# Performance work log

Measured on AMD Instinct MI355X. Metric: run time of the kernel, lower is better.

The kernel has to match this reference:

```python
import jax, jax.numpy as jnp
import numpy as np

B, S, D = 1, 2048, 2048
N_HEADS, N_KV_HEADS = 32, 8
HEAD_DIM = D // N_HEADS  # 64
N_REP = N_HEADS // N_KV_HEADS  # 4


def setup_inputs() -> dict:
    key = jax.random.key(0)
    ks = jax.random.split(key, 6)
    x = jax.random.normal(ks[0], (B, S, D), dtype=jnp.float32)
    # weights stored as [in, out] so projection is x @ W
    wq = jax.random.normal(ks[1], (D, N_HEADS * HEAD_DIM), dtype=jnp.float32) * 0.02
    wk = jax.random.normal(ks[2], (D, N_KV_HEADS * HEAD_DIM), dtype=jnp.float32) * 0.02
    wv = jax.random.normal(ks[3], (D, N_KV_HEADS * HEAD_DIM), dtype=jnp.float32) * 0.02
    wo = jax.random.normal(ks[4], (N_HEADS * HEAD_DIM, D), dtype=jnp.float32) * 0.02
    # RoPE tables: freqs_cis has shape (seqlen, head_dim//2)
    theta = 10000.0
    inv_freq = 1.0 / (theta ** (jnp.arange(0, HEAD_DIM, 2, dtype=jnp.float32) / HEAD_DIM))
    angles = jnp.arange(S, dtype=jnp.float32)[:, None] * inv_freq[None, :]  # [S, hd/2]
    freqs_cos = jnp.cos(angles)
    freqs_sin = jnp.sin(angles)
    # causal additive mask, broadcast to [b, h, q, k]
    mask = jnp.triu(jnp.full((S, S), -jnp.inf, dtype=jnp.float32), k=1)[None, None]
    return {"x": x, "wq": wq, "wk": wk, "wv": wv, "wo": wo,
            "freqs_cos": freqs_cos, "freqs_sin": freqs_sin, "mask": mask}


def _apply_rope(t, cos, sin):
    # t: [B, S, H, head_dim]; pairs (t[...,2i], t[...,2i+1]) form complex numbers
    tr = t[..., 0::2]
    ti = t[..., 1::2]
    c = cos[None, :, None, :]
    s = sin[None, :, None, :]
    out_r = tr * c - ti * s
    out_i = tr * s + ti * c
    return jnp.stack([out_r, out_i], axis=-1).reshape(t.shape)


def reference(x, wq, wk, wv, wo, freqs_cos, freqs_sin, mask):
    bsz, seqlen, _ = x.shape
    xq = (x @ wq).reshape(bsz, seqlen, N_HEADS, HEAD_DIM)
    xk = (x @ wk).reshape(bsz, seqlen, N_KV_HEADS, HEAD_DIM)
    xv = (x @ wv).reshape(bsz, seqlen, N_KV_HEADS, HEAD_DIM)
    xq = _apply_rope(xq, freqs_cos, freqs_sin)
    xk = _apply_rope(xk, freqs_cos, freqs_sin)
    # repeat_kv (GQA expansion): [b,s,kvh,d] -> [b,s,h,d]
    keys = jnp.repeat(xk, N_REP, axis=2)
    values = jnp.repeat(xv, N_REP, axis=2)
    scale = 1.0 / np.sqrt(HEAD_DIM)
    # scores: [b, h, q, k]
    scores = jnp.einsum('bqhd,bkhd->bhqk', xq, keys) * scale
    scores = scores + mask
    probs = jax.nn.softmax(scores.astype(jnp.float32), axis=-1).astype(x.dtype)
    out = jnp.einsum('bhqk,bkhd->bqhd', probs, values)
    out = out.reshape(bsz, seqlen, N_HEADS * HEAD_DIM)
    return out @ wo
```

## Files before the change

kernel.cpp:

```cpp
#include <hip/hip_runtime.h>
#include <hip/hip_bf16.h>

#define S_LEN 2048
#define D_MODEL 2048
#define N_HEADS 32
#define N_KV 8
#define HEAD_DIM 64
#define KV_DIM (N_KV * HEAD_DIM)
#define QKV_N (D_MODEL + 2 * KV_DIM)

typedef __bf16 bf16_t;
typedef __attribute__((ext_vector_type(8))) __bf16 bf16x8;
typedef __attribute__((ext_vector_type(4))) float f32x4;
typedef __attribute__((ext_vector_type(16))) float f32x16;
typedef __attribute__((ext_vector_type(4))) unsigned int uint4v;
typedef __attribute__((ext_vector_type(2))) unsigned int uint2v;

__device__ __forceinline__ void gload_lds16(const void* g, void* l) {
    __builtin_amdgcn_global_load_lds(
        (const __attribute__((address_space(1))) unsigned char*)g,
        (__attribute__((address_space(3))) unsigned char*)l,
        16, 0, 0);
}

__global__ __launch_bounds__(256) void transpose_convert(const float* __restrict__ src,
                                                         __hip_bfloat16* __restrict__ dst,
                                                         int R, int C) {
    __shared__ float tile[32][33];
    const int bx = blockIdx.x * 32;
    const int by = blockIdx.y * 32;
    const int tx = threadIdx.x;
    const int ty = threadIdx.y;
#pragma unroll
    for (int i = 0; i < 32; i += 8)
        tile[ty + i][tx] = src[(size_t)(by + ty + i) * C + bx + tx];
    __syncthreads();
#pragma unroll
    for (int i = 0; i < 32; i += 8)
        dst[(size_t)(bx + ty + i) * R + by + tx] = __float2bfloat16(tile[tx][ty + i]);
}

__global__ __launch_bounds__(256) void convert_bf16(const float* __restrict__ src,
                                                    __hip_bfloat16* __restrict__ dst) {
    const int i = (blockIdx.x * 256 + threadIdx.x) * 8;
    const float4 a = *reinterpret_cast<const float4*>(src + i);
    const float4 b = *reinterpret_cast<const float4*>(src + i + 4);
    bf16x8 r;
    r[0] = (__bf16)a.x; r[1] = (__bf16)a.y; r[2] = (__bf16)a.z; r[3] = (__bf16)a.w;
    r[4] = (__bf16)b.x; r[5] = (__bf16)b.y; r[6] = (__bf16)b.z; r[7] = (__bf16)b.w;
    *reinterpret_cast<bf16x8*>(dst + i) = r;
}

__global__ __launch_bounds__(256) void rope_qk(__hip_bfloat16* __restrict__ t,
                                               const float* __restrict__ cos_t,
                                               const float* __restrict__ sin_t) {
    const int idx = blockIdx.x * blockDim.x + threadIdx.x;
    const int i = idx & 31;
    const int hh = (idx >> 5) % (N_HEADS + N_KV);
    const int s = idx / (32 * (N_HEADS + N_KV));
    const float c = cos_t[s * 32 + i];
    const float sn = sin_t[s * 32 + i];
    int col; float scale;
    if (hh < N_HEADS) { col = hh * HEAD_DIM + 2 * i; scale = 0.125f * 1.44269504f; }
    else { col = D_MODEL + (hh - N_HEADS) * HEAD_DIM + 2 * i; scale = 1.0f; }
    __hip_bfloat16* p = &t[(size_t)s * QKV_N + col];
    const float re = __bfloat162float(p[0]);
    const float im = __bfloat162float(p[1]);
    p[0] = __float2bfloat16((re * c - im * sn) * scale);
    p[1] = __float2bfloat16((re * sn + im * c) * scale);
}

__global__ __launch_bounds__(256) void transpose_v(const __hip_bfloat16* __restrict__ QKV,
                                                   __hip_bfloat16* __restrict__ Vt) {
    __shared__ __align__(16) __bf16 tile[64][72];
    const int s0 = blockIdx.x * 64;
    const int hkv = blockIdx.y;
    const int tid = threadIdx.x;
    {
        const int r = tid >> 2;
        const int c0 = (tid & 3) * 16;
        const __hip_bfloat16* src = QKV + (size_t)(s0 + r) * QKV_N + D_MODEL + KV_DIM + hkv * HEAD_DIM + c0;
        *reinterpret_cast<bf16x8*>(&tile[r][c0]) = *reinterpret_cast<const bf16x8*>(src);
        *reinterpret_cast<bf16x8*>(&tile[r][c0 + 8]) = *reinterpret_cast<const bf16x8*>(src + 8);
    }
    __syncthreads();
    {
        const int d = tid >> 2;
        const int sc = (tid & 3) * 16;
        bf16x8 o0, o1;
#pragma unroll
        for (int j = 0; j < 8; ++j) { o0[j] = tile[sc + j][d]; o1[j] = tile[sc + 8 + j][d]; }
        __hip_bfloat16* dst = Vt + (size_t)(hkv * HEAD_DIM + d) * S_LEN + s0 + sc;
        *reinterpret_cast<bf16x8*>(dst) = o0;
        *reinterpret_cast<bf16x8*>(dst + 8) = o1;
    }
}

__device__ inline void storeC(__hip_bfloat16* p, float v) { *p = __float2bfloat16(v); }
__device__ inline void storeC(float* p, float v) { *p = v; }

template <typename OutT>
__global__ __launch_bounds__(256) void gemm_bt(const __hip_bfloat16* __restrict__ A,
                                               const __hip_bfloat16* __restrict__ Bt,
                                               OutT* __restrict__ C,
                                               int M, int N, int K) {
    __shared__ __align__(16) __bf16 As[2][128 * 32];
    __shared__ __align__(16) __bf16 Bs[2][128 * 32];
    const int tid = threadIdx.x;
    const int w = tid >> 6, l = tid & 63;
    const int wr = w >> 1, wc = w & 1;
    const int l4 = l >> 4, l15 = l & 15;
    const int bm = blockIdx.y * 128, bn = blockIdx.x * 128;

    f32x4 acc[4][4];
#pragma unroll
    for (int i = 0; i < 4; ++i)
#pragma unroll
        for (int j = 0; j < 4; ++j) acc[i][j] = (f32x4){0.f, 0.f, 0.f, 0.f};

    const int r0 = tid >> 2;
    const int cc0 = tid & 3;

    auto stage = [&](int buf, int k0) {
#pragma unroll
        for (int p = 0; p < 2; ++p) {
            const int row = p * 64 + r0;
            const int cs = cc0 ^ (row & 3);
            gload_lds16(&A[(size_t)(bm + row) * K + k0 + cs * 8], &As[buf][(p * 256 + tid) * 8]);
            gload_lds16(&Bt[(size_t)(bn + row) * K + k0 + cs * 8], &Bs[buf][(p * 256 + tid) * 8]);
        }
    };

    const int nk = K >> 5;
    stage(0, 0);
    asm volatile("s_waitcnt vmcnt(0)" ::: "memory");
    __builtin_amdgcn_s_barrier();

#pragma unroll 2
    for (int kt = 0; kt < nk; ++kt) {
        const int cur = kt & 1;
        if (kt + 1 < nk) stage(cur ^ 1, (kt + 1) * 32);
        bf16x8 a[4], b[4];
#pragma unroll
        for (int mi = 0; mi < 4; ++mi) {
            const int rr = wr * 64 + mi * 16 + l15;
            a[mi] = *reinterpret_cast<const bf16x8*>(&As[cur][rr * 32 + ((l4 ^ (rr & 3))) * 8]);
        }
#pragma unroll
        for (int ni = 0; ni < 4; ++ni) {
            const int rr = wc * 64 + ni * 16 + l15;
            b[ni] = *reinterpret_cast<const bf16x8*>(&Bs[cur][rr * 32 + ((l4 ^ (rr & 3))) * 8]);
        }
#pragma unroll
        for (int mi = 0; mi < 4; ++mi)
#pragma unroll
            for (int ni = 0; ni < 4; ++ni)
                acc[mi][ni] = __builtin_amdgcn_mfma_f32_16x16x32_bf16(a[mi], b[ni], acc[mi][ni], 0, 0, 0);
        asm volatile("s_waitcnt vmcnt(0)" ::: "memory");
        __builtin_amdgcn_s_barrier();
    }
#pragma unroll
    for (int mi = 0; mi < 4; ++mi)
#pragma unroll
        for (int ni = 0; ni < 4; ++ni)
#pragma unroll
            for (int r = 0; r < 4; ++r) {
                const int row = bm + wr * 64 + mi * 16 + l4 * 4 + r;
                const int col = bn + wc * 64 + ni * 16 + l15;
                storeC(&C[(size_t)row * N + col], acc[mi][ni][r]);
            }
}

__device__ __forceinline__ unsigned cvtpk_bf16(float lo, float hi) {
    unsigned w;
    asm("v_cvt_pk_bf16_f32 %0, %1, %2" : "=v"(w) : "v"(lo), "v"(hi));
    return w;
}
template <int R0>
__device__ __forceinline__ bf16x8 build_pfrag(const f32x16& s, int hi) {
    const unsigned A0 = cvtpk_bf16(s[R0 + 0], s[R0 + 1]);
    const unsigned A1 = cvtpk_bf16(s[R0 + 2], s[R0 + 3]);
    const unsigned B0 = cvtpk_bf16(s[R0 + 4], s[R0 + 5]);
    const unsigned B1 = cvtpk_bf16(s[R0 + 6], s[R0 + 7]);
    const unsigned pA0 = __shfl_xor(A0, 32, 64);
    const unsigned pA1 = __shfl_xor(A1, 32, 64);
    const unsigned pB0 = __shfl_xor(B0, 32, 64);
    const unsigned pB1 = __shfl_xor(B1, 32, 64);
    uint4v u;
    u[0] = hi ? pB0 : A0;
    u[1] = hi ? pB1 : A1;
    u[2] = hi ? B0 : pA0;
    u[3] = hi ? B1 : pA1;
    return __builtin_bit_cast(bf16x8, u);
}

__global__ __launch_bounds__(512) void attn_kernel(const __hip_bfloat16* __restrict__ QKV,
                                                   const __hip_bfloat16* __restrict__ Vt,
                                                   __hip_bfloat16* __restrict__ O,
                                                   float* __restrict__ Opart,
                                                   float* __restrict__ ms,
                                                   int split) {
    const int h = blockIdx.y;
    const int hkv = h >> 2;
    int qc = 0, sl = 0, gbase = 0, ns = 1;
    if (!split) {
        qc = 7 - (int)blockIdx.x;
    } else {
        const int x = (int)blockIdx.x;
        int cum = 0;
#pragma unroll
        for (int q = 0; q < 8; ++q) {
            const int n = (q + 2) >> 1;
            if (x >= cum && x < cum + n) { qc = q; sl = x - cum; gbase = cum; }
            cum += n;
        }
        ns = (qc + 2) >> 1;
    }
    const int ntf = 4 * (qc + 1);
    const int t0 = split ? sl * 8 : 0;
    const int t1 = split ? min(t0 + 8, ntf) : ntf;

    const int tid = threadIdx.x;
    const int w = tid >> 6, l = tid & 63;
    const int lq = l & 31, hi = l >> 5;
    const int q0w = qc * 256 + w * 32;
    const int qlane = q0w + lq;

    __shared__ __align__(16) __bf16 Ks[2][64 * 64];
    __shared__ __align__(16) __bf16 Vs[2][64 * 64];

    const __hip_bfloat16* Kg = QKV + D_MODEL + hkv * HEAD_DIM;
    const __hip_bfloat16* Vg = Vt + (size_t)hkv * HEAD_DIM * S_LEN;

    auto stage = [&](int buf, int kv0) {
        const int chunk = tid;
        const int r = chunk >> 3;
        const int cs = (chunk & 7) ^ (r & 7);
        gload_lds16(&Kg[(size_t)(kv0 + r) * QKV_N + cs * 8], &Ks[buf][chunk * 8]);
        gload_lds16(&Vg[(size_t)r * S_LEN + kv0 + cs * 8], &Vs[buf][chunk * 8]);
    };

    bf16x8 qf[4];
#pragma unroll
    for (int f = 0; f < 4; ++f)
        qf[f] = *reinterpret_cast<const bf16x8*>(
            &QKV[(size_t)qlane * QKV_N + h * HEAD_DIM + 16 * f + 8 * hi]);

    f32x16 o0, o1;
#pragma unroll
    for (int r = 0; r < 16; ++r) { o0[r] = 0.f; o1[r] = 0.f; }
    float m_run = -__builtin_inff(), s_run = 0.f;

    stage(0, t0 * 64);

#pragma unroll 1
    for (int t = t0; t < t1; ++t) {
        __syncthreads();
        if (t + 1 < t1) stage((t + 1 - t0) & 1, (t + 1) * 64);
        const int kv0 = t * 64;
        if (kv0 <= q0w + 31) {
            const __bf16* Kb = Ks[(t - t0) & 1];
            const __bf16* Vb = Vs[(t - t0) & 1];

            f32x16 s0, s1;
#pragma unroll
            for (int r = 0; r < 16; ++r) { s0[r] = 0.f; s1[r] = 0.f; }
#pragma unroll
            for (int f = 0; f < 4; ++f) {
                const int rr0 = lq;
                const int rr1 = 32 + lq;
                const bf16x8 ka0 = *reinterpret_cast<const bf16x8*>(
                    &Kb[rr0 * 64 + (((2 * f + hi) ^ (rr0 & 7))) * 8]);
                const bf16x8 ka1 = *reinterpret_cast<const bf16x8*>(
                    &Kb[rr1 * 64 + (((2 * f + hi) ^ (rr1 & 7))) * 8]);
                s0 = __builtin_amdgcn_mfma_f32_32x32x16_bf16(ka0, qf[f], s0, 0, 0, 0);
                s1 = __builtin_amdgcn_mfma_f32_32x32x16_bf16(ka1, qf[f], s1, 0, 0, 0);
            }
            if (kv0 + 63 > q0w) {
#pragma unroll
                for (int r = 0; r < 16; ++r) {
                    const int kvb = (r & 3) + 8 * (r >> 2) + 4 * hi;
                    if (kv0 + kvb > qlane) s0[r] = -__builtin_inff();
                    if (kv0 + 32 + kvb > qlane) s1[r] = -__builtin_inff();
                }
            }
            float ta = fmaxf(s0[0], s1[0]), tb = fmaxf(s0[1], s1[1]);
            float tc = fmaxf(s0[2], s1[2]), td = fmaxf(s0[3], s1[3]);
#pragma unroll
            for (int r = 4; r < 16; r += 4) {
                ta = fmaxf(ta, fmaxf(s0[r], s1[r]));
                tb = fmaxf(tb, fmaxf(s0[r + 1], s1[r + 1]));
                tc = fmaxf(tc, fmaxf(s0[r + 2], s1[r + 2]));
                td = fmaxf(td, fmaxf(s0[r + 3], s1[r + 3]));
            }
            float m_row = fmaxf(fmaxf(ta, tb), fmaxf(tc, td));
            m_row = fmaxf(m_row, __shfl_xor(m_row, 32, 64));

            if (!__all(m_row <= m_run + 8.0f)) {
                const float mnew = fmaxf(m_run, m_row);
                const float corr = exp2f(m_run - mnew);
                m_run = mnew;
                s_run *= corr;
#pragma unroll
                for (int r = 0; r < 16; ++r) { o0[r] *= corr; o1[r] *= corr; }
            }
#pragma unroll
            for (int r = 0; r < 16; ++r) {
                s0[r] = exp2f(s0[r] - m_run);
                s1[r] = exp2f(s1[r] - m_run);
            }
            float ua = s0[0] + s1[0], ub = s0[1] + s1[1];
            float uc = s0[2] + s1[2], ud = s0[3] + s1[3];
#pragma unroll
            for (int r = 4; r < 16; r += 4) {
                ua += s0[r] + s1[r];
                ub += s0[r + 1] + s1[r + 1];
                uc += s0[r + 2] + s1[r + 2];
                ud += s0[r + 3] + s1[r + 3];
            }
            float rs = (ua + ub) + (uc + ud);
            rs += __shfl_xor(rs, 32, 64);
            s_run += rs;

            bf16x8 pa[4];
            pa[0] = build_pfrag<0>(s0, hi);
            pa[1] = build_pfrag<8>(s0, hi);
            pa[2] = build_pfrag<0>(s1, hi);
            pa[3] = build_pfrag<8>(s1, hi);

#pragma unroll
            for (int ks = 0; ks < 4; ++ks) {
                const int rv0 = lq;
                const int rv1 = 32 + lq;
                const bf16x8 va0 = *reinterpret_cast<const bf16x8*>(
                    &Vb[rv0 * 64 + (((2 * ks + hi) ^ (rv0 & 7))) * 8]);
                const bf16x8 va1 = *reinterpret_cast<const bf16x8*>(
                    &Vb[rv1 * 64 + (((2 * ks + hi) ^ (rv1 & 7))) * 8]);
                o0 = __builtin_amdgcn_mfma_f32_32x32x16_bf16(va0, pa[ks], o0, 0, 0, 0);
                o1 = __builtin_amdgcn_mfma_f32_32x32x16_bf16(va1, pa[ks], o1, 0, 0, 0);
            }
        }
    }

    if (ns == 1) {
        const float inv = 1.0f / s_run;
        __hip_bfloat16* orow = O + (size_t)qlane * D_MODEL + h * HEAD_DIM;
#pragma unroll
        for (int rr = 0; rr < 4; ++rr) {
            {
                uint2v u;
                u[0] = cvtpk_bf16(o0[4 * rr] * inv, o0[4 * rr + 1] * inv);
                u[1] = cvtpk_bf16(o0[4 * rr + 2] * inv, o0[4 * rr + 3] * inv);
                *reinterpret_cast<uint2v*>(orow + 8 * rr + 4 * hi) = u;
            }
            {
                uint2v u;
                u[0] = cvtpk_bf16(o1[4 * rr] * inv, o1[4 * rr + 1] * inv);
                u[1] = cvtpk_bf16(o1[4 * rr + 2] * inv, o1[4 * rr + 3] * inv);
                *reinterpret_cast<uint2v*>(orow + 32 + 8 * rr + 4 * hi) = u;
            }
        }
    } else {
        const int g = h * 20 + gbase + sl;
        const int row = w * 32 + lq;
        const size_t base = ((size_t)g * 256 + row) * 64;
#pragma unroll
        for (int rr = 0; rr < 4; ++rr) {
            f32x4 v0, v1;
#pragma unroll
            for (int j = 0; j < 4; ++j) { v0[j] = o0[4 * rr + j]; v1[j] = o1[4 * rr + j]; }
            *reinterpret_cast<f32x4*>(&Opart[base + 8 * rr + 4 * hi]) = v0;
            *reinterpret_cast<f32x4*>(&Opart[base + 32 + 8 * rr + 4 * hi]) = v1;
        }
        if (hi == 0) {
            const size_t mi = (size_t)g * 256 + row;
            ms[mi * 2] = m_run;
            ms[mi * 2 + 1] = s_run;
        }
    }
}

__device__ __constant__ int kCum[8] = {0, 1, 2, 4, 6, 9, 12, 16};

__global__ __launch_bounds__(256) void attn_merge(const float* __restrict__ Opart,
                                                  const float* __restrict__ ms,
                                                  __hip_bfloat16* __restrict__ O) {
    const int qc = 2 + blockIdx.x;
    const int h = blockIdx.z;
    const int tid = threadIdx.x;
    const int row = blockIdx.y * 32 + (tid >> 3);
    const int dv0 = (tid & 7) * 8;
    const int ns = (qc + 2) >> 1;
    const int g0 = h * 20 + kCum[qc];

    float mv[4], sv[4];
    float M = -__builtin_inff();
#pragma unroll
    for (int s = 0; s < 4; ++s) {
        if (s < ns) {
            const size_t mi = (size_t)(g0 + s) * 256 + row;
            mv[s] = ms[mi * 2];
            sv[s] = ms[mi * 2 + 1];
            M = fmaxf(M, mv[s]);
        }
    }
    float S = 0.f;
    float acc[8];
#pragma unroll
    for (int j = 0; j < 8; ++j) acc[j] = 0.f;
#pragma unroll
    for (int s = 0; s < 4; ++s) {
        if (s < ns) {
            const float wgt = exp2f(mv[s] - M);
            S += wgt * sv[s];
            const float* p = &Opart[((size_t)(g0 + s) * 256 + row) * 64 + dv0];
            const float4 a = *reinterpret_cast<const float4*>(p);
            const float4 b = *reinterpret_cast<const float4*>(p + 4);
            acc[0] += wgt * a.x; acc[1] += wgt * a.y; acc[2] += wgt * a.z; acc[3] += wgt * a.w;
            acc[4] += wgt * b.x; acc[5] += wgt * b.y; acc[6] += wgt * b.z; acc[7] += wgt * b.w;
        }
    }
    const float inv = 1.0f / S;
    uint4v u;
    u[0] = cvtpk_bf16(acc[0] * inv, acc[1] * inv);
    u[1] = cvtpk_bf16(acc[2] * inv, acc[3] * inv);
    u[2] = cvtpk_bf16(acc[4] * inv, acc[5] * inv);
    u[3] = cvtpk_bf16(acc[6] * inv, acc[7] * inv);
    *reinterpret_cast<uint4v*>(&O[(size_t)(qc * 256 + row) * D_MODEL + h * HEAD_DIM + dv0]) = u;
}

extern "C" void kernel_launch(void* const* d_in, const int* in_sizes, int n_in,
                              void* d_out, int out_size, void* d_ws, size_t ws_size,
                              hipStream_t stream) {
    const float* x  = (const float*)d_in[0];
    const float* wq = (const float*)d_in[1];
    const float* wk = (const float*)d_in[2];
    const float* wv = (const float*)d_in[3];
    const float* wo = (const float*)d_in[4];
    const float* fc = (const float*)d_in[5];
    const float* fs = (const float*)d_in[6];
    float* out = (float*)d_out;

    char* ws = (char*)d_ws;
    __hip_bfloat16* wqkvT = (__hip_bfloat16*)(ws);
    __hip_bfloat16* woT   = (__hip_bfloat16*)(ws + (12u << 20));
    __hip_bfloat16* attnb = (__hip_bfloat16*)(ws + (20u << 20));
    __hip_bfloat16* xb    = (__hip_bfloat16*)(ws + (28u << 20));
    __hip_bfloat16* QKV   = (__hip_bfloat16*)(ws + (36u << 20));
    __hip_bfloat16* Vt    = (__hip_bfloat16*)(ws + (48u << 20));
    float*          msb   = (float*)(ws + (50u << 20));
    float*          Opart = (float*)(ws + (53u << 20));

    const int split = (ws_size >= (96ull << 20)) ? 1 : 0;

    const dim3 tb(32, 8);
    transpose_convert<<<dim3(D_MODEL / 32, D_MODEL / 32), tb, 0, stream>>>(wq, wqkvT, D_MODEL, D_MODEL);
    transpose_convert<<<dim3(KV_DIM / 32, D_MODEL / 32), tb, 0, stream>>>(wk, wqkvT + (size_t)D_MODEL * D_MODEL, D_MODEL, KV_DIM);
    transpose_convert<<<dim3(KV_DIM / 32, D_MODEL / 32), tb, 0, stream>>>(wv, wqkvT + (size_t)(D_MODEL + KV_DIM) * D_MODEL, D_MODEL, KV_DIM);
    transpose_convert<<<dim3(D_MODEL / 32, D_MODEL / 32), tb, 0, stream>>>(wo, woT, D_MODEL, D_MODEL);
    convert_bf16<<<(S_LEN * D_MODEL) / (256 * 8), 256, 0, stream>>>(x, xb);

    gemm_bt<__hip_bfloat16><<<dim3(QKV_N / 128, S_LEN / 128), 256, 0, stream>>>(xb, wqkvT, QKV, S_LEN, QKV_N, D_MODEL);

    rope_qk<<<(S_LEN * (N_HEADS + N_KV) * 32) / 256, 256, 0, stream>>>(QKV, fc, fs);

    transpose_v<<<dim3(S_LEN / 64, N_KV), 256, 0, stream>>>(QKV, Vt);

    if (split) {
        attn_kernel<<<dim3(20, N_HEADS), 512, 0, stream>>>(QKV, Vt, attnb, Opart, msb, 1);
        attn_merge<<<dim3(6, 8, N_HEADS), 256, 0, stream>>>(Opart, msb, attnb);
    } else {
        attn_kernel<<<dim3(8, N_HEADS), 512, 0, stream>>>(QKV, Vt, attnb, Opart, msb, 0);
    }

    gemm_bt<float><<<dim3(D_MODEL / 128, S_LEN / 128), 256, 0, stream>>>(attnb, woT, out, S_LEN, D_MODEL, D_MODEL);

    (void)in_sizes; (void)n_in; (void)out_size;
}
```

Before: 176.1 us.

## Widen attention KV tiles to 128 with causal sub-tile skipping and bf16 partials

The attention kernel now stages 128-key K/V tiles per iteration instead of 64, which halves the number of barriers and loop iterations. Within a tile, 32-key sub-blocks lying fully above the causal diagonal skip their QK and PV MFMAs. MFMA sections are wrapped in s_setprio. Split-KV partial outputs are stored as bf16 rather than fp32, which halves partial-output traffic in the attention and merge kernels. In exchange, LDS use doubles (64KB), which may reduce occupancy, and the partials lose precision.

```diff
diff --git a/kernel.cpp b/kernel.cpp
--- a/kernel.cpp
+++ b/kernel.cpp
@@ -197,7 +197,7 @@
 __global__ __launch_bounds__(512) void attn_kernel(const __hip_bfloat16* __restrict__ QKV,
                                                    const __hip_bfloat16* __restrict__ Vt,
                                                    __hip_bfloat16* __restrict__ O,
-                                                   float* __restrict__ Opart,
+                                                   __hip_bfloat16* __restrict__ Opart,
                                                    float* __restrict__ ms,
                                                    int split) {
     const int h = blockIdx.y;
@@ -216,28 +216,34 @@
         }
         ns = (qc + 2) >> 1;
     }
-    const int ntf = 4 * (qc + 1);
-    const int t0 = split ? sl * 8 : 0;
-    const int t1 = split ? min(t0 + 8, ntf) : ntf;
+    const int nph = 2 * (qc + 1);
+    const int ph0 = split ? sl * 4 : 0;
+    const int ph1 = split ? min(ph0 + 4, nph) : nph;
 
     const int tid = threadIdx.x;
     const int w = tid >> 6, l = tid & 63;
     const int lq = l & 31, hi = l >> 5;
+    const int sx = lq & 7;
     const int q0w = qc * 256 + w * 32;
     const int qlane = q0w + lq;
 
-    __shared__ __align__(16) __bf16 Ks[2][64 * 64];
-    __shared__ __align__(16) __bf16 Vs[2][64 * 64];
+    __shared__ __align__(16) __bf16 Ks[2][128 * 64];
+    __shared__ __align__(16) __bf16 Vs[2][64 * 128];
 
     const __hip_bfloat16* Kg = QKV + D_MODEL + hkv * HEAD_DIM;
     const __hip_bfloat16* Vg = Vt + (size_t)hkv * HEAD_DIM * S_LEN;
 
     auto stage = [&](int buf, int kv0) {
-        const int chunk = tid;
-        const int r = chunk >> 3;
-        const int cs = (chunk & 7) ^ (r & 7);
-        gload_lds16(&Kg[(size_t)(kv0 + r) * QKV_N + cs * 8], &Ks[buf][chunk * 8]);
-        gload_lds16(&Vg[(size_t)r * S_LEN + kv0 + cs * 8], &Vs[buf][chunk * 8]);
+#pragma unroll
+        for (int pp = 0; pp < 2; ++pp) {
+            const int ck = tid + pp * 512;
+            const int rk = ck >> 3;
+            const int csk = (ck & 7) ^ (rk & 7);
+            gload_lds16(&Kg[(size_t)(kv0 + rk) * QKV_N + csk * 8], &Ks[buf][ck * 8]);
+            const int rv = ck >> 4;
+            const int csv = (ck & 15) ^ (rv & 7);
+            gload_lds16(&Vg[(size_t)rv * S_LEN + kv0 + csv * 8], &Vs[buf][ck * 8]);
+        }
     };
 
     bf16x8 qf[4];
@@ -251,47 +257,84 @@
     for (int r = 0; r < 16; ++r) { o0[r] = 0.f; o1[r] = 0.f; }
     float m_run = -__builtin_inff(), s_run = 0.f;
 
-    stage(0, t0 * 64);
+    stage(0, ph0 * 128);
+
+#define QK_SUB(sv, C)                                                              \
+    do {                                                                           \
+        _Pragma("unroll")                                                          \
+        for (int f = 0; f < 4; ++f) {                                              \
+            const bf16x8 ka = *reinterpret_cast<const bf16x8*>(                    \
+                &Kb[(32 * (C) + lq) * 64 + (((2 * f + hi) ^ sx)) * 8]);            \
+            sv = __builtin_amdgcn_mfma_f32_32x32x16_bf16(ka, qf[f], sv, 0, 0, 0);  \
+        }                                                                          \
+    } while (0)
+
+#define PV_SUB(sv, C)                                                              \
+    do {                                                                           \
+        const bf16x8 paA = build_pfrag<0>(sv, hi);                                 \
+        const bf16x8 vA0 = *reinterpret_cast<const bf16x8*>(                       \
+            &Vb[lq * 128 + (((4 * (C) + hi) ^ sx)) * 8]);                          \
+        const bf16x8 vA1 = *reinterpret_cast<const bf16x8*>(                       \
+            &Vb[(32 + lq) * 128 + (((4 * (C) + hi) ^ sx)) * 8]);                   \
+        o0 = __builtin_amdgcn_mfma_f32_32x32x16_bf16(vA0, paA, o0, 0, 0, 0);       \
+        o1 = __builtin_amdgcn_mfma_f32_32x32x16_bf16(vA1, paA, o1, 0, 0, 0);       \
+        const bf16x8 paB = build_pfrag<8>(sv, hi);                                 \
+        const bf16x8 vB0 = *reinterpret_cast<const bf16x8*>(                       \
+            &Vb[lq * 128 + (((4 * (C) + 2 + hi) ^ sx)) * 8]);                      \
+        const bf16x8 vB1 = *reinterpret_cast<const bf16x8*>(                       \
+            &Vb[(32 + lq) * 128 + (((4 * (C) + 2 + hi) ^ sx)) * 8]);               \
+        o0 = __builtin_amdgcn_mfma_f32_32x32x16_bf16(vB0, paB, o0, 0, 0, 0);       \
+        o1 = __builtin_amdgcn_mfma_f32_32x32x16_bf16(vB1, paB, o1, 0, 0, 0);       \
+    } while (0)
 
 #pragma unroll 1
-    for (int t = t0; t < t1; ++t) {
+    for (int p = ph0; p < ph1; ++p) {
         __syncthreads();
-        if (t + 1 < t1) stage((t + 1 - t0) & 1, (t + 1) * 64);
-        const int kv0 = t * 64;
+        if (p + 1 < ph1) stage((p + 1 - ph0) & 1, (p + 1) * 128);
+        const int kv0 = p * 128;
         if (kv0 <= q0w + 31) {
-            const __bf16* Kb = Ks[(t - t0) & 1];
-            const __bf16* Vb = Vs[(t - t0) & 1];
-
-            f32x16 s0, s1;
-#pragma unroll
-            for (int r = 0; r < 16; ++r) { s0[r] = 0.f; s1[r] = 0.f; }
-#pragma unroll
-            for (int f = 0; f < 4; ++f) {
-                const int rr0 = lq;
-                const int rr1 = 32 + lq;
-                const bf16x8 ka0 = *reinterpret_cast<const bf16x8*>(
-                    &Kb[rr0 * 64 + (((2 * f + hi) ^ (rr0 & 7))) * 8]);
-                const bf16x8 ka1 = *reinterpret_cast<const bf16x8*>(
-                    &Kb[rr1 * 64 + (((2 * f + hi) ^ (rr1 & 7))) * 8]);
-                s0 = __builtin_amdgcn_mfma_f32_32x32x16_bf16(ka0, qf[f], s0, 0, 0, 0);
-                s1 = __builtin_amdgcn_mfma_f32_32x32x16_bf16(ka1, qf[f], s1, 0, 0, 0);
-            }
-            if (kv0 + 63 > q0w) {
+            const __bf16* Kb = Ks[(p - ph0) & 1];
+            const __bf16* Vb = Vs[(p - ph0) & 1];
+            const bool v1 = (kv0 + 32 <= q0w + 31);
+            const bool v2 = (kv0 + 64 <= q0w + 31);
+            const bool v3 = (kv0 + 96 <= q0w + 31);
+
+            f32x16 s0, s1, s2, s3;
+            const float NI = -__builtin_inff();
+#pragma unroll
+            for (int r = 0; r < 16; ++r) {
+                s0[r] = 0.f;
+                s1[r] = v1 ? 0.f : NI;
+                s2[r] = v2 ? 0.f : NI;
+                s3[r] = v3 ? 0.f : NI;
+            }
+            __builtin_amdgcn_s_setprio(1);
+            QK_SUB(s0, 0);
+            if (v1) QK_SUB(s1, 1);
+            if (v2) QK_SUB(s2, 2);
+            if (v3) QK_SUB(s3, 3);
+            __builtin_amdgcn_s_setprio(0);
+
+            if (kv0 + 127 > q0w) {
 #pragma unroll
                 for (int r = 0; r < 16; ++r) {
                     const int kvb = (r & 3) + 8 * (r >> 2) + 4 * hi;
-                    if (kv0 + kvb > qlane) s0[r] = -__builtin_inff();
-                    if (kv0 + 32 + kvb > qlane) s1[r] = -__builtin_inff();
+                    if (kv0 + kvb > qlane) s0[r] = NI;
+                    if (kv0 + 32 + kvb > qlane) s1[r] = NI;
+                    if (kv0 + 64 + kvb > qlane) s2[r] = NI;
+                    if (kv0 + 96 + kvb > qlane) s3[r] = NI;
                 }
             }
-            float ta = fmaxf(s0[0], s1[0]), tb = fmaxf(s0[1], s1[1]);
-            float tc = fmaxf(s0[2], s1[2]), td = fmaxf(s0[3], s1[3]);
+            float ta = fmaxf(fmaxf(s0[0], s1[0]), fmaxf(s2[0], s3[0]));
+            float tb = fmaxf(fmaxf(s0[1], s1[1]), fmaxf(s2[1], s3[1]));
+            float tc = fmaxf(fmaxf(s0[2], s1[2]), fmaxf(s2[2], s3[2]));
+            float td = fmaxf(fmaxf(s0[3], s1[3]), fmaxf(s2[3], s3[3]));
 #pragma unroll
             for (int r = 4; r < 16; r += 4) {
-                ta = fmaxf(ta, fmaxf(s0[r], s1[r]));
-                tb = fmaxf(tb, fmaxf(s0[r + 1], s1[r + 1]));
-                tc = fmaxf(tc, fmaxf(s0[r + 2], s1[r + 2]));
-                td = fmaxf(td, fmaxf(s0[r + 3], s1[r + 3]));
+                ta = fmaxf(ta, fmaxf(fmaxf(s0[r], s1[r]), fmaxf(s2[r], s3[r])));
+                tb = fmaxf(tb, fmaxf(fmaxf(s0[r + 1], s1[r + 1]), fmaxf(s2[r + 1], s3[r + 1])));
+                tc = fmaxf(tc, fmaxf(fmaxf(s0[r + 2], s1[r + 2]), fmaxf(s2[r + 2], s3[r + 2])));
+                td = fmaxf(td, fmaxf(fmaxf(s0[r + 3], s1[r + 3]), fmaxf(s2[r + 3], s3[r + 3])));
             }
             float m_row = fmaxf(fmaxf(ta, tb), fmaxf(tc, td));
             m_row = fmaxf(m_row, __shfl_xor(m_row, 32, 64));
@@ -308,39 +351,34 @@
             for (int r = 0; r < 16; ++r) {
                 s0[r] = exp2f(s0[r] - m_run);
                 s1[r] = exp2f(s1[r] - m_run);
-            }
-            float ua = s0[0] + s1[0], ub = s0[1] + s1[1];
-            float uc = s0[2] + s1[2], ud = s0[3] + s1[3];
+                s2[r] = exp2f(s2[r] - m_run);
+                s3[r] = exp2f(s3[r] - m_run);
+            }
+            float ua = s0[0] + s1[0] + s2[0] + s3[0];
+            float ub = s0[1] + s1[1] + s2[1] + s3[1];
+            float uc = s0[2] + s1[2] + s2[2] + s3[2];
+            float ud = s0[3] + s1[3] + s2[3] + s3[3];
 #pragma unroll
             for (int r = 4; r < 16; r += 4) {
-                ua += s0[r] + s1[r];
-                ub += s0[r + 1] + s1[r + 1];
-                uc += s0[r + 2] + s1[r + 2];
-                ud += s0[r + 3] + s1[r + 3];
+                ua += s0[r] + s1[r] + s2[r] + s3[r];
+                ub += s0[r + 1] + s1[r + 1] + s2[r + 1] + s3[r + 1];
+                uc += s0[r + 2] + s1[r + 2] + s2[r + 2] + s3[r + 2];
+                ud += s0[r + 3] + s1[r + 3] + s2[r + 3] + s3[r + 3];
             }
             float rs = (ua + ub) + (uc + ud);
             rs += __shfl_xor(rs, 32, 64);
             s_run += rs;
 
-            bf16x8 pa[4];
-            pa[0] = build_pfrag<0>(s0, hi);
-            pa[1] = build_pfrag<8>(s0, hi);
-            pa[2] = build_pfrag<0>(s1, hi);
-            pa[3] = build_pfrag<8>(s1, hi);
-
-#pragma unroll
-            for (int ks = 0; ks < 4; ++ks) {
-                const int rv0 = lq;
-                const int rv1 = 32 + lq;
-                const bf16x8 va0 = *reinterpret_cast<const bf16x8*>(
-                    &Vb[rv0 * 64 + (((2 * ks + hi) ^ (rv0 & 7))) * 8]);
-                const bf16x8 va1 = *reinterpret_cast<const bf16x8*>(
-                    &Vb[rv1 * 64 + (((2 * ks + hi) ^ (rv1 & 7))) * 8]);
-                o0 = __builtin_amdgcn_mfma_f32_32x32x16_bf16(va0, pa[ks], o0, 0, 0, 0);
-                o1 = __builtin_amdgcn_mfma_f32_32x32x16_bf16(va1, pa[ks], o1, 0, 0, 0);
-            }
-        }
-    }
+            __builtin_amdgcn_s_setprio(1);
+            PV_SUB(s0, 0);
+            if (v1) PV_SUB(s1, 1);
+            if (v2) PV_SUB(s2, 2);
+            if (v3) PV_SUB(s3, 3);
+            __builtin_amdgcn_s_setprio(0);
+        }
+    }
+#undef QK_SUB
+#undef PV_SUB
 
     if (ns == 1) {
         const float inv = 1.0f / s_run;
@@ -363,14 +401,21 @@
     } else {
         const int g = h * 20 + gbase + sl;
         const int row = w * 32 + lq;
-        const size_t base = ((size_t)g * 256 + row) * 64;
+        __hip_bfloat16* pb = Opart + ((size_t)g * 256 + row) * 64;
 #pragma unroll
         for (int rr = 0; rr < 4; ++rr) {
-            f32x4 v0, v1;
-#pragma unroll
-            for (int j = 0; j < 4; ++j) { v0[j] = o0[4 * rr + j]; v1[j] = o1[4 * rr + j]; }
-            *reinterpret_cast<f32x4*>(&Opart[base + 8 * rr + 4 * hi]) = v0;
-            *reinterpret_cast<f32x4*>(&Opart[base + 32 + 8 * rr + 4 * hi]) = v1;
+            {
+                uint2v u;
+                u[0] = cvtpk_bf16(o0[4 * rr], o0[4 * rr + 1]);
+                u[1] = cvtpk_bf16(o0[4 * rr + 2], o0[4 * rr + 3]);
+                *reinterpret_cast<uint2v*>(pb + 8 * rr + 4 * hi) = u;
+            }
+            {
+                uint2v u;
+                u[0] = cvtpk_bf16(o1[4 * rr], o1[4 * rr + 1]);
+                u[1] = cvtpk_bf16(o1[4 * rr + 2], o1[4 * rr + 3]);
+                *reinterpret_cast<uint2v*>(pb + 32 + 8 * rr + 4 * hi) = u;
+            }
         }
         if (hi == 0) {
             const size_t mi = (size_t)g * 256 + row;
@@ -382,7 +427,7 @@
 
 __device__ __constant__ int kCum[8] = {0, 1, 2, 4, 6, 9, 12, 16};
 
-__global__ __launch_bounds__(256) void attn_merge(const float* __restrict__ Opart,
+__global__ __launch_bounds__(256) void attn_merge(const __hip_bfloat16* __restrict__ Opart,
                                                   const float* __restrict__ ms,
                                                   __hip_bfloat16* __restrict__ O) {
     const int qc = 2 + blockIdx.x;
@@ -413,11 +458,10 @@
         if (s < ns) {
             const float wgt = exp2f(mv[s] - M);
             S += wgt * sv[s];
-            const float* p = &Opart[((size_t)(g0 + s) * 256 + row) * 64 + dv0];
-            const float4 a = *reinterpret_cast<const float4*>(p);
-            const float4 b = *reinterpret_cast<const float4*>(p + 4);
-            acc[0] += wgt * a.x; acc[1] += wgt * a.y; acc[2] += wgt * a.z; acc[3] += wgt * a.w;
-            acc[4] += wgt * b.x; acc[5] += wgt * b.y; acc[6] += wgt * b.z; acc[7] += wgt * b.w;
+            const bf16x8 v = *reinterpret_cast<const bf16x8*>(
+                &Opart[((size_t)(g0 + s) * 256 + row) * 64 + dv0]);
+#pragma unroll
+            for (int j = 0; j < 8; ++j) acc[j] += wgt * (float)v[j];
         }
     }
     const float inv = 1.0f / S;
@@ -449,9 +493,9 @@
     __hip_bfloat16* QKV   = (__hip_bfloat16*)(ws + (36u << 20));
     __hip_bfloat16* Vt    = (__hip_bfloat16*)(ws + (48u << 20));
     float*          msb   = (float*)(ws + (50u << 20));
-    float*          Opart = (float*)(ws + (53u << 20));
-
-    const int split = (ws_size >= (96ull << 20)) ? 1 : 0;
+    __hip_bfloat16* Opart = (__hip_bfloat16*)(ws + (53u << 20));
+
+    const int split = (ws_size >= (80ull << 20)) ? 1 : 0;
 
     const dim3 tb(32, 8);
     transpose_convert<<<dim3(D_MODEL / 32, D_MODEL / 32), tb, 0, stream>>>(wq, wqkvT, D_MODEL, D_MODEL);
```

Measured after the change: 182.5 us. 1.04x slower.
